# Kernel tuning notes

Measured on AMD Instinct MI355X. Metric: run time of the kernel, lower is better.

The kernel has to match this reference:

```python
import jax, jax.numpy as jnp
import numpy as np

B, S, D, H = 2, 4096, 512, 8
HD = D // H  # head_dim = 64


def _rope_cache(s, d, base=10000.0):
    half = d // 2
    inv_freq = 1.0 / base ** (jnp.arange(half, dtype=jnp.float32) / half)
    t = jnp.arange(s, dtype=jnp.float32)
    freqs = jnp.einsum('s,d->sd', t, inv_freq)          # [s, half]
    emb = jnp.concatenate([freqs, freqs], axis=-1)      # [s, d]
    return jnp.cos(emb), jnp.sin(emb)


def _rotate_half(x):
    x1, x2 = jnp.split(x, 2, axis=-1)
    return jnp.concatenate([-x2, x1], axis=-1)


def setup_inputs() -> dict:
    key = jax.random.key(0)
    k1, k2, k3 = jax.random.split(key, 3)
    x = jax.random.normal(k1, (B, S, D), dtype=jnp.float32)
    W_qkv = jax.random.normal(k2, (D, 3 * D), dtype=jnp.float32) * (D ** -0.5)
    W_out = jax.random.normal(k3, (D, D), dtype=jnp.float32) * (D ** -0.5)
    # causal mask [B, S, S] (True = attend), exercises the masking branch
    causal = jnp.tril(jnp.ones((S, S), dtype=bool))
    attention_mask = jnp.broadcast_to(causal, (B, S, S))
    return {"x": x, "W_qkv": W_qkv, "W_out": W_out, "attention_mask": attention_mask}


def reference(x, W_qkv, W_out, attention_mask):
    b, s, d = x.shape
    qkv = x @ W_qkv                                     # [b, s, 3d]
    q, k, v = jnp.split(qkv, 3, axis=-1)

    def split_heads(t):
        return t.reshape(b, s, H, HD).transpose(0, 2, 1, 3)  # [b, h, s, hd]

    q, k, v = map(split_heads, (q, k, v))
    cos, sin = _rope_cache(s, HD)                       # [s, hd]
    cos = cos[None, None]                               # [1, 1, s, hd]
    sin = sin[None, None]
    q = q * cos + _rotate_half(q) * sin
    k = k * cos + _rotate_half(k) * sin

    scale = HD ** -0.5
    logits = jnp.einsum('bhid,bhjd->bhij', q, k) * scale
    logits = jnp.where(attention_mask[:, None, :, :], logits, jnp.float32(-1e9))
    attn = jax.nn.softmax(logits, axis=-1)
    out = jnp.einsum('bhij,bhjd->bhid', attn, v)
    out = out.transpose(0, 2, 1, 3).reshape(b, s, d)
    return out @ W_out
```

## Files before the change

kernel.cpp:

```cpp
#include <hip/hip_runtime.h>
#include <hip/hip_bf16.h>

typedef __attribute__((ext_vector_type(8))) short bf16x8;
typedef __attribute__((ext_vector_type(4))) float f32x4;
typedef __attribute__((ext_vector_type(16))) float f32x16;
typedef __attribute__((ext_vector_type(4))) unsigned int u32x4;

#define AS3(p)  ((__attribute__((address_space(3))) unsigned int*)(p))
#define AS1C(p) ((const __attribute__((address_space(1))) unsigned int*)(p))

__device__ __forceinline__ ushort f2b(float f){
  __hip_bfloat16 h = __float2bfloat16(f);
  return *reinterpret_cast<ushort*>(&h);
}
__device__ __forceinline__ float b2f(ushort u){
  unsigned int x = ((unsigned int)u) << 16;
  return __uint_as_float(x);
}
__device__ __forceinline__ unsigned int packbf(float lo, float hi){
  return ((unsigned int)f2b(hi) << 16) | (unsigned int)f2b(lo);
}

__device__ __forceinline__ int sniff_f32(const ushort* __restrict__ x, int flat){
  int l = flat & 63;
  float a = b2f(x[l]),     b = b2f(x[l+64]);
  float c = b2f(x[l+128]), d = b2f(x[l+192]);
  int bad = (!(fabsf(a) < 1e6f)) || (!(fabsf(b) < 1e6f)) ||
            (!(fabsf(c) < 1e6f)) || (!(fabsf(d) < 1e6f));
  return __ballot(bad) != 0ULL;
}

__global__ __launch_bounds__(256) void prep(
    const void* __restrict__ x, ushort* __restrict__ xb,
    const void* __restrict__ Wqkv, ushort* __restrict__ WqkvT,
    const void* __restrict__ Wout, ushort* __restrict__ WoutT,
    float* __restrict__ tc, float* __restrict__ ts){
  __shared__ ushort t[32][33];
  const int bid = blockIdx.x, tid = threadIdx.x;
  if (bid < 512){
    int i = bid*256 + tid;
    int s = i >> 5, d = i & 31;
    float inv = powf(10000.0f, -(float)d * (1.0f/32.0f));
    float a = (float)s * inv;
    tc[i] = cosf(a);
    ts[i] = sinf(a);
  } else if (bid < 2560){
    const int isf = sniff_f32((const ushort*)x, tid);
    const int n = 2*4096*512;
    int i = (bid-512)*256 + tid;
    const int stride = 2048*256;
    if (isf){ const float* s = (const float*)x;  for (; i<n; i+=stride) xb[i] = f2b(s[i]); }
    else    { const ushort* s = (const ushort*)x; for (; i<n; i+=stride) xb[i] = s[i]; }
  } else {
    const int isf = sniff_f32((const ushort*)x, tid);
    const void* in; ushort* out; int R, C, bx, by;
    if (bid < 3328){ int q = bid-2560; in = Wqkv; out = WqkvT; R = 512; C = 1536; bx = q%48; by = q/48; }
    else           { int q = bid-3328; in = Wout; out = WoutT; R = 512; C = 512;  bx = q%16; by = q/16; }
    int c0 = bx*32, r0 = by*32;
    int tx = tid&31, ty = tid>>5;
#pragma unroll
    for (int r=0;r<32;r+=8){
      size_t idx = (size_t)(r0+ty+r)*C + c0+tx;
      t[ty+r][tx] = isf ? f2b(((const float*)in)[idx]) : ((const ushort*)in)[idx];
    }
    __syncthreads();
#pragma unroll
    for (int r=0;r<32;r+=8) out[(size_t)(c0+ty+r)*R + r0+tx] = t[tx][ty+r];
  }
}

__global__ __launch_bounds__(256, 2) void qkv_rope(
    const ushort* __restrict__ X, const ushort* __restrict__ WT,
    const float* __restrict__ tc, const float* __restrict__ ts,
    ushort* __restrict__ Q, ushort* __restrict__ Ko, ushort* __restrict__ VT){
  __shared__ __align__(16) ushort Al[128*64];
  __shared__ __align__(16) ushort Bl[128*64];
  __shared__ __align__(16) ushort Tl[64*136];
  const int w = threadIdx.x>>6, lane = threadIdx.x&63;
  const int n0 = blockIdx.x*128, m0 = blockIdx.y*128;
  f32x4 acc[4][4] = {};
  const ushort* Ag = X  + (size_t)m0*512;
  const ushort* Bg = WT + (size_t)n0*512;
  const int srow = lane>>3, sphys = lane&7;
  for (int k0=0;k0<512;k0+=64){
#pragma unroll
    for (int tt=0;tt<4;tt++){
      int r = tt*32 + w*8 + srow;
      int lc = sphys ^ (r&7);
      __builtin_amdgcn_global_load_lds(AS1C(Ag + (size_t)r*512 + k0 + lc*8), AS3(Al + (tt*32+w*8)*64), 16, 0, 0);
      __builtin_amdgcn_global_load_lds(AS1C(Bg + (size_t)r*512 + k0 + lc*8), AS3(Bl + (tt*32+w*8)*64), 16, 0, 0);
    }
    __syncthreads();
    const int mh = (w>>1)*64, nh = (w&1)*64;
#pragma unroll
    for (int kk=0;kk<2;kk++){
      bf16x8 af[4], bf[4];
#pragma unroll
      for (int mt=0;mt<4;mt++){
        int r = mh + mt*16 + (lane&15);
        int pc = (kk*4 + (lane>>4)) ^ (r&7);
        af[mt] = *(const bf16x8*)(Al + r*64 + pc*8);
      }
#pragma unroll
      for (int nt=0;nt<4;nt++){
        int r = nh + nt*16 + (lane&15);
        int pc = (kk*4 + (lane>>4)) ^ (r&7);
        bf[nt] = *(const bf16x8*)(Bl + r*64 + pc*8);
      }
#pragma unroll
      for (int mt=0;mt<4;mt++)
#pragma unroll
        for (int nt=0;nt<4;nt++)
          acc[mt][nt] = __builtin_amdgcn_mfma_f32_16x16x32_bf16(af[mt], bf[nt], acc[mt][nt], 0,0,0);
    }
    __syncthreads();
  }
  const int c = lane & 15;
  const int rbase = m0 + (w>>1)*64 + (lane>>4)*4;
  if (n0 < 1024){
    const int colbase = n0 + (w&1)*64;
    const int sec = colbase >> 9;
    const int h = (colbase & 511) >> 6;
    const float scale = (sec==0) ? 0.125f : 1.0f;
    ushort* Out = (sec==0) ? Q : Ko;
#pragma unroll
    for (int mt=0;mt<4;mt++){
#pragma unroll
      for (int reg=0;reg<4;reg++){
        int rg = rbase + mt*16 + reg;
        int b = rg>>12, s = rg&4095;
        size_t obase = ((size_t)(b*8+h)*4096 + s)*64;
        const float* tcp = tc + s*32;
        const float* tsp = ts + s*32;
#pragma unroll
        for (int nt=0;nt<2;nt++){
          int d1 = nt*16 + c;
          float cv = tcp[d1], sv = tsp[d1];
          float v1 = acc[mt][nt][reg], v2 = acc[mt][nt+2][reg];
          Out[obase + d1]      = f2b(scale*(v1*cv - v2*sv));
          Out[obase + d1 + 32] = f2b(scale*(v2*cv + v1*sv));
        }
      }
    }
  } else {
    const int M = w>>1, P = w&1;
    const int bb = m0>>12, s0 = m0&4095;
    const int dR = threadIdx.x>>4, sj = threadIdx.x&15;
#pragma unroll
    for (int ph=0; ph<2; ph++){
      if (P == ph){
#pragma unroll
        for (int mt=0;mt<4;mt++)
#pragma unroll
          for (int nt=0;nt<4;nt++){
            ushort4 pk;
            pk.x = f2b(acc[mt][nt][0]);
            pk.y = f2b(acc[mt][nt][1]);
            pk.z = f2b(acc[mt][nt][2]);
            pk.w = f2b(acc[mt][nt][3]);
            *(ushort4*)&Tl[(nt*16+c)*136 + M*64 + mt*16 + (lane>>4)*4] = pk;
          }
      }
      __syncthreads();
      const int hh = ((n0 + ph*64) & 511) >> 6;
      ushort* baseV = VT + ((size_t)(bb*8+hh)*64)*4096 + s0;
#pragma unroll
      for (int pass=0; pass<4; pass++){
        int d = pass*16 + dR;
        *(u32x4*)(baseV + (size_t)d*4096 + sj*8) = *(const u32x4*)&Tl[d*136 + sj*8];
      }
      __syncthreads();
    }
  }
}

__global__ __launch_bounds__(256, 2) void flash_attn(
    const ushort* __restrict__ Q, const ushort* __restrict__ K,
    const ushort* __restrict__ V, ushort* __restrict__ O,
    ushort* __restrict__ Opart, float* __restrict__ Lpart){
  __shared__ __align__(16) ushort Kl[2][128*64];
  __shared__ __align__(16) ushort Vl[2][64*128];
  const int w = threadIdx.x>>6, lane = threadIdx.x&63;
  const int ln = lane&31, half = lane>>5;
  const int z = blockIdx.x;
  const int bh = (z&7)*2 + ((z>>3)&1);
  const int t = z>>4;
  int qi, jlo, jhi, mode, slot = 0;
  if (t < 16){ qi = 15 - t; jlo = 0; jhi = qi; mode = 0; }
  else {
    int u = t - 16; qi = 31 - (u>>1); int hf = u&1;
    int h1 = (qi+1) >> 1;
    jlo = hf ? h1 : 0; jhi = hf ? qi : h1-1; mode = 1;
    slot = (bh*16 + (qi-16))*2 + hf;
  }
  const int q0 = qi*128;
  const int qg = q0 + w*32 + ln;
  const ushort* Qb = Q + (size_t)bh*4096*64;
  const ushort* Kb = K + (size_t)bh*4096*64;
  const ushort* Vb = V + (size_t)bh*4096*64;
  bf16x8 qf[4];
#pragma unroll
  for (int kt=0;kt<4;kt++)
    qf[kt] = *(const bf16x8*)(Qb + (size_t)qg*64 + kt*16 + half*8);
  f32x16 oacc[2] = {};
  float lsum = 0.0f;
  const int krow = lane>>3, kchunk = lane&7;
  const int vrow = lane>>4, vchunk = lane&15;
  auto stage = [&](int j, int b){
    const int k0 = j*128;
    ushort* Kd = &Kl[b][0];
    ushort* Vd = &Vl[b][0];
#pragma unroll
    for (int tt=0;tt<4;tt++){
      int rr = (w*4+tt)*8 + krow;
      int kc = kchunk ^ (rr&7);
      __builtin_amdgcn_global_load_lds(AS1C(Kb + (size_t)(k0+rr)*64 + kc*8),
                                       AS3(Kd + (w*4+tt)*8*64), 16, 0, 0);
      int dd = (w*4+tt)*4 + vrow;
      int vc = vchunk ^ (dd&7);
      __builtin_amdgcn_global_load_lds(AS1C(Vb + (size_t)dd*4096 + k0 + vc*8),
                                       AS3(Vd + (w*4+tt)*4*128), 16, 0, 0);
    }
  };
  stage(jlo, 0);
  int cur = 0;
  for (int j=jlo; j<=jhi; j++){
    __syncthreads();
    if (j < jhi) stage(j+1, cur^1);
    const ushort* Kc = &Kl[cur][0];
    const ushort* Vc = &Vl[cur][0];
    const int k0 = j*128;
    const bool diag = (j==qi);
#pragma unroll
    for (int nt=0;nt<4;nt++){
      f32x16 s_ = {};
#pragma unroll
      for (int kt=0;kt<4;kt++){
        int kr = nt*32+ln;
        int p = (kt*2+half) ^ (kr&7);
        bf16x8 kf = *(const bf16x8*)(Kc + kr*64 + p*8);
        s_ = __builtin_amdgcn_mfma_f32_32x32x16_bf16(kf, qf[kt], s_, 0,0,0);
      }
      float pv[16];
      const int kb = k0 + nt*32 + 4*half;
      if (diag){
#pragma unroll
        for (int qd=0;qd<4;qd++)
#pragma unroll
          for (int e=0;e<4;e++){
            float sv = s_[4*qd+e];
            if ((kb + 8*qd + e) > qg) sv = -1e30f;
            pv[4*qd+e] = __expf(fminf(sv, 30.0f));
          }
      } else {
#pragma unroll
        for (int qd=0;qd<4;qd++)
#pragma unroll
          for (int e=0;e<4;e++)
            pv[4*qd+e] = __expf(fminf(s_[4*qd+e], 30.0f));
      }
      unsigned int qk[8];
#pragma unroll
      for (int qd=0;qd<4;qd++){
        lsum += pv[4*qd] + pv[4*qd+1] + pv[4*qd+2] + pv[4*qd+3];
        qk[2*qd]   = packbf(pv[4*qd],   pv[4*qd+1]);
        qk[2*qd+1] = packbf(pv[4*qd+2], pv[4*qd+3]);
      }
#pragma unroll
      for (int khi=0;khi<2;khi++){
        unsigned int keep0 = half ? qk[4*khi+2] : qk[4*khi+0];
        unsigned int keep1 = half ? qk[4*khi+3] : qk[4*khi+1];
        unsigned int send0 = half ? qk[4*khi+0] : qk[4*khi+2];
        unsigned int send1 = half ? qk[4*khi+1] : qk[4*khi+3];
        unsigned int r0 = (unsigned int)__shfl_xor((int)send0, 32);
        unsigned int r1 = (unsigned int)__shfl_xor((int)send1, 32);
        union { unsigned int u[4]; bf16x8 v; } pf;
        pf.u[0] = half ? r0 : keep0;
        pf.u[1] = half ? r1 : keep1;
        pf.u[2] = half ? keep0 : r0;
        pf.u[3] = half ? keep1 : r1;
        const int cl = (nt*2+khi)*2 + half;
#pragma unroll
        for (int dt=0;dt<2;dt++){
          int vr = dt*32+ln;
          int p = cl ^ (vr&7);
          bf16x8 vf = *(const bf16x8*)(Vc + vr*128 + p*8);
          oacc[dt] = __builtin_amdgcn_mfma_f32_32x32x16_bf16(pf.v, vf, oacc[dt], 0,0,0);
        }
      }
    }
    cur ^= 1;
  }
  if (mode == 0){
    float linv = 1.0f / (lsum + __shfl_xor(lsum, 32));
    const int b = bh>>3, h = bh&7;
#pragma unroll
    for (int reg=0;reg<16;reg++){
      int qlocal = (reg&3) + 8*(reg>>2) + 4*half;
      float li = __shfl(linv, qlocal);
      int srw = q0 + w*32 + qlocal;
#pragma unroll
      for (int dt=0;dt<2;dt++)
        O[((size_t)(b*4096+srw))*512 + h*64 + dt*32 + ln] = f2b(oacc[dt][reg]*li);
    }
  } else {
    ushort* Ob = Opart + (size_t)slot*8192;
#pragma unroll
    for (int reg=0;reg<16;reg++){
      int qlocal = (reg&3) + 8*(reg>>2) + 4*half;
      int r = w*32 + qlocal;
#pragma unroll
      for (int dt=0;dt<2;dt++)
        Ob[r*64 + dt*32 + ln] = f2b(oacc[dt][reg]);
    }
    float lrow = lsum + __shfl_xor(lsum, 32);
    if (half == 0) Lpart[slot*128 + w*32 + ln] = lrow;
  }
}

__global__ __launch_bounds__(256) void combine(
    const ushort* __restrict__ Opart, const float* __restrict__ Lpart,
    ushort* __restrict__ O){
  const int qq = blockIdx.x;
  const int bh = blockIdx.y;
  const int slot0 = (bh*16 + qq)*2;
  const ushort* O1 = Opart + (size_t)slot0*8192;
  const ushort* O2 = O1 + 8192;
  const float*  L1 = Lpart + slot0*128;
  const float*  L2 = L1 + 128;
  const int b = bh>>3, h = bh&7;
  const int s0 = (16+qq)*128;
  const int r0 = threadIdx.x>>2, cg = (threadIdx.x&3)*16;
#pragma unroll
  for (int it=0; it<2; it++){
    int r = r0 + it*64;
    float li = 1.0f / (L1[r] + L2[r]);
    ushort* dst = O + ((size_t)(b*4096 + s0 + r))*512 + h*64 + cg;
    const ushort* p1 = O1 + r*64 + cg;
    const ushort* p2 = O2 + r*64 + cg;
#pragma unroll
    for (int e=0;e<16;e++)
      dst[e] = f2b((b2f(p1[e]) + b2f(p2[e])) * li);
  }
}

__global__ __launch_bounds__(256, 2) void out_proj(
    const ushort* __restrict__ A, const ushort* __restrict__ WT,
    void* __restrict__ Out, const ushort* __restrict__ xs){
  __shared__ __align__(16) ushort Al[128*64];
  __shared__ __align__(16) ushort Bl[128*64];
  const int isf = sniff_f32(xs, threadIdx.x);
  const int w = threadIdx.x>>6, lane = threadIdx.x&63;
  const int n0 = blockIdx.x*128, m0 = blockIdx.y*128;
  f32x4 acc[4][4] = {};
  const ushort* Ag = A  + (size_t)m0*512;
  const ushort* Bg = WT + (size_t)n0*512;
  const int srow = lane>>3, sphys = lane&7;
  for (int k0=0;k0<512;k0+=64){
#pragma unroll
    for (int tt=0;tt<4;tt++){
      int r = tt*32 + w*8 + srow;
      int lc = sphys ^ (r&7);
      __builtin_amdgcn_global_load_lds(AS1C(Ag + (size_t)r*512 + k0 + lc*8), AS3(Al + (tt*32+w*8)*64), 16, 0, 0);
      __builtin_amdgcn_global_load_lds(AS1C(Bg + (size_t)r*512 + k0 + lc*8), AS3(Bl + (tt*32+w*8)*64), 16, 0, 0);
    }
    __syncthreads();
    const int mh = (w>>1)*64, nh = (w&1)*64;
#pragma unroll
    for (int kk=0;kk<2;kk++){
      bf16x8 af[4], bf[4];
#pragma unroll
      for (int mt=0;mt<4;mt++){
        int r = mh + mt*16 + (lane&15);
        int pc = (kk*4 + (lane>>4)) ^ (r&7);
        af[mt] = *(const bf16x8*)(Al + r*64 + pc*8);
      }
#pragma unroll
      for (int nt=0;nt<4;nt++){
        int r = nh + nt*16 + (lane&15);
        int pc = (kk*4 + (lane>>4)) ^ (r&7);
        bf[nt] = *(const bf16x8*)(Bl + r*64 + pc*8);
      }
#pragma unroll
      for (int mt=0;mt<4;mt++)
#pragma unroll
        for (int nt=0;nt<4;nt++)
          acc[mt][nt] = __builtin_amdgcn_mfma_f32_16x16x32_bf16(af[mt], bf[nt], acc[mt][nt], 0,0,0);
    }
    __syncthreads();
  }
  const int c = lane&15;
  const int rbase = m0 + (w>>1)*64 + (lane>>4)*4;
  const int cb = n0 + (w&1)*64;
#pragma unroll
  for (int mt=0;mt<4;mt++)
#pragma unroll
    for (int nt=0;nt<4;nt++)
#pragma unroll
      for (int reg=0;reg<4;reg++){
        int rg = rbase + mt*16 + reg;
        size_t idx = (size_t)rg*512 + cb + nt*16 + c;
        float v = acc[mt][nt][reg];
        if (isf) ((float*)Out)[idx] = v;
        else     ((ushort*)Out)[idx] = f2b(v);
      }
}

extern "C" void kernel_launch(void* const* d_in, const int* in_sizes, int n_in,
                              void* d_out, int out_size, void* d_ws, size_t ws_size,
                              hipStream_t stream){
  const void* x    = d_in[0];
  const void* Wqkv = d_in[1];
  const void* Wout = d_in[2];
  char* ws = (char*)d_ws;
  float*  tc    = (float*) (ws + 4096);
  float*  tsn   = (float*) (ws + 528384);
  ushort* WqkvT = (ushort*)(ws + 1052672);
  ushort* WoutT = (ushort*)(ws + 2625536);
  ushort* xb    = (ushort*)(ws + 3149824);
  ushort* Qw    = (ushort*)(ws + 11538432);
  ushort* Kw    = (ushort*)(ws + 19927040);
  ushort* Vw    = (ushort*)(ws + 28315648);
  ushort* Ow    = (ushort*)(ws + 36704256);
  ushort* Opart = xb;
  float*  Lpart = tc;

  prep     <<<dim3(3584),  dim3(256), 0, stream>>>(x, xb, Wqkv, WqkvT, Wout, WoutT, tc, tsn);
  qkv_rope <<<dim3(12,64), dim3(256), 0, stream>>>(xb, WqkvT, tc, tsn, Qw, Kw, Vw);
  flash_attn<<<dim3(768),  dim3(256), 0, stream>>>(Qw, Kw, Vw, Ow, Opart, Lpart);
  combine  <<<dim3(16,16), dim3(256), 0, stream>>>(Opart, Lpart, Ow);
  out_proj <<<dim3(4,64),  dim3(256), 0, stream>>>(Ow, WoutT, d_out, (const ushort*)x);
}
```

Baseline: 288.3 us.

## Compute RoPE inline, shrink attention KV tiles, use exp2 softmax, raise occupancy

Drops the precomputed cos/sin tables and instead evaluates RoPE in the QKV epilogue with hardware sin/cos on fractional turns. Folds log2(e) into the Q scale so the softmax can use exp2 without clamping. Halves the flash-attention K/V tile to 64 keys, which cuts LDS use and allows a higher occupancy hint, and the P operand no longer needs cross-lane shuffles. The bf16 pack now uses a simpler rounding path, and launch bounds are raised on the GEMMs. The risks are register spills from the higher occupancy targets, twice as many loop iterations, and slightly different rounding in the RoPE angles and the packed probabilities.

```diff
diff --git a/kernel.cpp b/kernel.cpp
--- a/kernel.cpp
+++ b/kernel.cpp
@@ -17,8 +17,10 @@
   unsigned int x = ((unsigned int)u) << 16;
   return __uint_as_float(x);
 }
-__device__ __forceinline__ unsigned int packbf(float lo, float hi){
-  return ((unsigned int)f2b(hi) << 16) | (unsigned int)f2b(lo);
+__device__ __forceinline__ unsigned int pack_rn(float lo, float hi){
+  unsigned int a = __float_as_uint(lo) + 0x8000u;
+  unsigned int b = __float_as_uint(hi) + 0x8000u;
+  return __builtin_amdgcn_perm(b, a, 0x07060302u);
 }
 
 __device__ __forceinline__ int sniff_f32(const ushort* __restrict__ x, int flat){
@@ -33,29 +35,21 @@
 __global__ __launch_bounds__(256) void prep(
     const void* __restrict__ x, ushort* __restrict__ xb,
     const void* __restrict__ Wqkv, ushort* __restrict__ WqkvT,
-    const void* __restrict__ Wout, ushort* __restrict__ WoutT,
-    float* __restrict__ tc, float* __restrict__ ts){
+    const void* __restrict__ Wout, ushort* __restrict__ WoutT){
   __shared__ ushort t[32][33];
   const int bid = blockIdx.x, tid = threadIdx.x;
-  if (bid < 512){
-    int i = bid*256 + tid;
-    int s = i >> 5, d = i & 31;
-    float inv = powf(10000.0f, -(float)d * (1.0f/32.0f));
-    float a = (float)s * inv;
-    tc[i] = cosf(a);
-    ts[i] = sinf(a);
-  } else if (bid < 2560){
+  if (bid < 2048){
     const int isf = sniff_f32((const ushort*)x, tid);
     const int n = 2*4096*512;
-    int i = (bid-512)*256 + tid;
+    int i = bid*256 + tid;
     const int stride = 2048*256;
     if (isf){ const float* s = (const float*)x;  for (; i<n; i+=stride) xb[i] = f2b(s[i]); }
     else    { const ushort* s = (const ushort*)x; for (; i<n; i+=stride) xb[i] = s[i]; }
   } else {
     const int isf = sniff_f32((const ushort*)x, tid);
     const void* in; ushort* out; int R, C, bx, by;
-    if (bid < 3328){ int q = bid-2560; in = Wqkv; out = WqkvT; R = 512; C = 1536; bx = q%48; by = q/48; }
-    else           { int q = bid-3328; in = Wout; out = WoutT; R = 512; C = 512;  bx = q%16; by = q/16; }
+    if (bid < 2816){ int q = bid-2048; in = Wqkv; out = WqkvT; R = 512; C = 1536; bx = q%48; by = q/48; }
+    else           { int q = bid-2816; in = Wout; out = WoutT; R = 512; C = 512;  bx = q%16; by = q/16; }
     int c0 = bx*32, r0 = by*32;
     int tx = tid&31, ty = tid>>5;
 #pragma unroll
@@ -69,9 +63,8 @@
   }
 }
 
-__global__ __launch_bounds__(256, 2) void qkv_rope(
+__global__ __launch_bounds__(256, 3) void qkv_rope(
     const ushort* __restrict__ X, const ushort* __restrict__ WT,
-    const float* __restrict__ tc, const float* __restrict__ ts,
     ushort* __restrict__ Q, ushort* __restrict__ Ko, ushort* __restrict__ VT){
   __shared__ __align__(16) ushort Al[128*64];
   __shared__ __align__(16) ushort Bl[128*64];
@@ -121,8 +114,12 @@
     const int colbase = n0 + (w&1)*64;
     const int sec = colbase >> 9;
     const int h = (colbase & 511) >> 6;
-    const float scale = (sec==0) ? 0.125f : 1.0f;
+    const float scale = (sec==0) ? 0.125f*1.44269504089f : 1.0f;
     ushort* Out = (sec==0) ? Q : Ko;
+    float invr[2];
+#pragma unroll
+    for (int nt=0;nt<2;nt++)
+      invr[nt] = __builtin_amdgcn_exp2f(-0.415241011861f * (float)(nt*16 + c)) * 0.159154943092f;
 #pragma unroll
     for (int mt=0;mt<4;mt++){
 #pragma unroll
@@ -130,12 +127,13 @@
         int rg = rbase + mt*16 + reg;
         int b = rg>>12, s = rg&4095;
         size_t obase = ((size_t)(b*8+h)*4096 + s)*64;
-        const float* tcp = tc + s*32;
-        const float* tsp = ts + s*32;
+        float sf = (float)s;
 #pragma unroll
         for (int nt=0;nt<2;nt++){
+          float fr = __builtin_amdgcn_fractf(sf * invr[nt]);
+          float cv = __builtin_amdgcn_cosf(fr);
+          float sv = __builtin_amdgcn_sinf(fr);
           int d1 = nt*16 + c;
-          float cv = tcp[d1], sv = tsp[d1];
           float v1 = acc[mt][nt][reg], v2 = acc[mt][nt+2][reg];
           Out[obase + d1]      = f2b(scale*(v1*cv - v2*sv));
           Out[obase + d1 + 32] = f2b(scale*(v2*cv + v1*sv));
@@ -174,23 +172,22 @@
   }
 }
 
-__global__ __launch_bounds__(256, 2) void flash_attn(
+__global__ __launch_bounds__(256, 4) void flash_attn(
     const ushort* __restrict__ Q, const ushort* __restrict__ K,
     const ushort* __restrict__ V, ushort* __restrict__ O,
     ushort* __restrict__ Opart, float* __restrict__ Lpart){
-  __shared__ __align__(16) ushort Kl[2][128*64];
-  __shared__ __align__(16) ushort Vl[2][64*128];
+  __shared__ __align__(16) ushort Kl[2][64*64];
+  __shared__ __align__(16) ushort Vl[2][64*64];
   const int w = threadIdx.x>>6, lane = threadIdx.x&63;
   const int ln = lane&31, half = lane>>5;
   const int z = blockIdx.x;
   const int bh = (z&7)*2 + ((z>>3)&1);
   const int t = z>>4;
   int qi, jlo, jhi, mode, slot = 0;
-  if (t < 16){ qi = 15 - t; jlo = 0; jhi = qi; mode = 0; }
+  if (t < 16){ qi = 15 - t; jlo = 0; jhi = 2*qi+1; mode = 0; }
   else {
     int u = t - 16; qi = 31 - (u>>1); int hf = u&1;
-    int h1 = (qi+1) >> 1;
-    jlo = hf ? h1 : 0; jhi = hf ? qi : h1-1; mode = 1;
+    jlo = hf ? (qi+1) : 0; jhi = hf ? (2*qi+1) : qi; mode = 1;
     slot = (bh*16 + (qi-16))*2 + hf;
   }
   const int q0 = qi*128;
@@ -204,22 +201,19 @@
     qf[kt] = *(const bf16x8*)(Qb + (size_t)qg*64 + kt*16 + half*8);
   f32x16 oacc[2] = {};
   float lsum = 0.0f;
-  const int krow = lane>>3, kchunk = lane&7;
-  const int vrow = lane>>4, vchunk = lane&15;
+  const int r8 = lane>>3, sl = lane&7;
   auto stage = [&](int j, int b){
-    const int k0 = j*128;
+    const int k0 = j*64;
     ushort* Kd = &Kl[b][0];
     ushort* Vd = &Vl[b][0];
 #pragma unroll
-    for (int tt=0;tt<4;tt++){
-      int rr = (w*4+tt)*8 + krow;
-      int kc = kchunk ^ (rr&7);
-      __builtin_amdgcn_global_load_lds(AS1C(Kb + (size_t)(k0+rr)*64 + kc*8),
-                                       AS3(Kd + (w*4+tt)*8*64), 16, 0, 0);
-      int dd = (w*4+tt)*4 + vrow;
-      int vc = vchunk ^ (dd&7);
-      __builtin_amdgcn_global_load_lds(AS1C(Vb + (size_t)dd*4096 + k0 + vc*8),
-                                       AS3(Vd + (w*4+tt)*4*128), 16, 0, 0);
+    for (int tt=0;tt<2;tt++){
+      int rr = w*16 + tt*8 + r8;
+      int lc = sl ^ (rr&7);
+      __builtin_amdgcn_global_load_lds(AS1C(Kb + (size_t)(k0+rr)*64 + lc*8),
+                                       AS3(Kd + (w*16+tt*8)*64), 16, 0, 0);
+      __builtin_amdgcn_global_load_lds(AS1C(Vb + (size_t)rr*4096 + k0 + lc*8),
+                                       AS3(Vd + (w*16+tt*8)*64), 16, 0, 0);
     }
   };
   stage(jlo, 0);
@@ -229,10 +223,10 @@
     if (j < jhi) stage(j+1, cur^1);
     const ushort* Kc = &Kl[cur][0];
     const ushort* Vc = &Vl[cur][0];
-    const int k0 = j*128;
-    const bool diag = (j==qi);
-#pragma unroll
-    for (int nt=0;nt<4;nt++){
+    const int k0 = j*64;
+    const bool dm = (k0 + 63) > (q0 + w*32);
+#pragma unroll
+    for (int nt=0;nt<2;nt++){
       f32x16 s_ = {};
 #pragma unroll
       for (int kt=0;kt<4;kt++){
@@ -241,51 +235,40 @@
         bf16x8 kf = *(const bf16x8*)(Kc + kr*64 + p*8);
         s_ = __builtin_amdgcn_mfma_f32_32x32x16_bf16(kf, qf[kt], s_, 0,0,0);
       }
+      const int kb = k0 + nt*32 + 4*half;
       float pv[16];
-      const int kb = k0 + nt*32 + 4*half;
-      if (diag){
-#pragma unroll
-        for (int qd=0;qd<4;qd++)
-#pragma unroll
-          for (int e=0;e<4;e++){
-            float sv = s_[4*qd+e];
-            if ((kb + 8*qd + e) > qg) sv = -1e30f;
-            pv[4*qd+e] = __expf(fminf(sv, 30.0f));
-          }
+      if (dm){
+#pragma unroll
+        for (int r=0;r<16;r++){
+          int kk = kb + 8*(r>>2) + (r&3);
+          pv[r] = (kk > qg) ? 0.0f : __builtin_amdgcn_exp2f(s_[r]);
+        }
       } else {
 #pragma unroll
-        for (int qd=0;qd<4;qd++)
-#pragma unroll
-          for (int e=0;e<4;e++)
-            pv[4*qd+e] = __expf(fminf(s_[4*qd+e], 30.0f));
+        for (int r=0;r<16;r++) pv[r] = __builtin_amdgcn_exp2f(s_[r]);
       }
       unsigned int qk[8];
 #pragma unroll
       for (int qd=0;qd<4;qd++){
-        lsum += pv[4*qd] + pv[4*qd+1] + pv[4*qd+2] + pv[4*qd+3];
-        qk[2*qd]   = packbf(pv[4*qd],   pv[4*qd+1]);
-        qk[2*qd+1] = packbf(pv[4*qd+2], pv[4*qd+3]);
+        lsum += (pv[4*qd]+pv[4*qd+1]) + (pv[4*qd+2]+pv[4*qd+3]);
+        qk[2*qd]   = pack_rn(pv[4*qd],   pv[4*qd+1]);
+        qk[2*qd+1] = pack_rn(pv[4*qd+2], pv[4*qd+3]);
       }
 #pragma unroll
       for (int khi=0;khi<2;khi++){
-        unsigned int keep0 = half ? qk[4*khi+2] : qk[4*khi+0];
-        unsigned int keep1 = half ? qk[4*khi+3] : qk[4*khi+1];
-        unsigned int send0 = half ? qk[4*khi+0] : qk[4*khi+2];
-        unsigned int send1 = half ? qk[4*khi+1] : qk[4*khi+3];
-        unsigned int r0 = (unsigned int)__shfl_xor((int)send0, 32);
-        unsigned int r1 = (unsigned int)__shfl_xor((int)send1, 32);
         union { unsigned int u[4]; bf16x8 v; } pf;
-        pf.u[0] = half ? r0 : keep0;
-        pf.u[1] = half ? r1 : keep1;
-        pf.u[2] = half ? keep0 : r0;
-        pf.u[3] = half ? keep1 : r1;
-        const int cl = (nt*2+khi)*2 + half;
+        pf.u[0] = qk[khi*4+0]; pf.u[1] = qk[khi*4+1];
+        pf.u[2] = qk[khi*4+2]; pf.u[3] = qk[khi*4+3];
+        const int c0 = nt*4 + khi*2;
 #pragma unroll
         for (int dt=0;dt<2;dt++){
           int vr = dt*32+ln;
-          int p = cl ^ (vr&7);
-          bf16x8 vf = *(const bf16x8*)(Vc + vr*128 + p*8);
-          oacc[dt] = __builtin_amdgcn_mfma_f32_32x32x16_bf16(pf.v, vf, oacc[dt], 0,0,0);
+          int pc0 = c0 ^ (vr&7);
+          int pc1 = (c0+1) ^ (vr&7);
+          union { unsigned int u[4]; bf16x8 v; } vf;
+          *(uint2*)&vf.u[0] = *(const uint2*)(Vc + vr*64 + pc0*8 + half*4);
+          *(uint2*)&vf.u[2] = *(const uint2*)(Vc + vr*64 + pc1*8 + half*4);
+          oacc[dt] = __builtin_amdgcn_mfma_f32_32x32x16_bf16(pf.v, vf.v, oacc[dt], 0,0,0);
         }
       }
     }
@@ -344,7 +327,7 @@
   }
 }
 
-__global__ __launch_bounds__(256, 2) void out_proj(
+__global__ __launch_bounds__(256, 4) void out_proj(
     const ushort* __restrict__ A, const ushort* __restrict__ WT,
     void* __restrict__ Out, const ushort* __restrict__ xs){
   __shared__ __align__(16) ushort Al[128*64];
@@ -413,8 +396,7 @@
   const void* Wqkv = d_in[1];
   const void* Wout = d_in[2];
   char* ws = (char*)d_ws;
-  float*  tc    = (float*) (ws + 4096);
-  float*  tsn   = (float*) (ws + 528384);
+  float*  Lpart = (float*) (ws + 4096);
   ushort* WqkvT = (ushort*)(ws + 1052672);
   ushort* WoutT = (ushort*)(ws + 2625536);
   ushort* xb    = (ushort*)(ws + 3149824);
@@ -423,10 +405,9 @@
   ushort* Vw    = (ushort*)(ws + 28315648);
   ushort* Ow    = (ushort*)(ws + 36704256);
   ushort* Opart = xb;
-  float*  Lpart = tc;
-
-  prep     <<<dim3(3584),  dim3(256), 0, stream>>>(x, xb, Wqkv, WqkvT, Wout, WoutT, tc, tsn);
-  qkv_rope <<<dim3(12,64), dim3(256), 0, stream>>>(xb, WqkvT, tc, tsn, Qw, Kw, Vw);
+
+  prep     <<<dim3(3072),  dim3(256), 0, stream>>>(x, xb, Wqkv, WqkvT, Wout, WoutT);
+  qkv_rope <<<dim3(12,64), dim3(256), 0, stream>>>(xb, WqkvT, Qw, Kw, Vw);
   flash_attn<<<dim3(768),  dim3(256), 0, stream>>>(Qw, Kw, Vw, Ow, Opart, Lpart);
   combine  <<<dim3(16,16), dim3(256), 0, stream>>>(Opart, Lpart, Ow);
   out_proj <<<dim3(4,64),  dim3(256), 0, stream>>>(Ow, WoutT, d_out, (const ushort*)x);
```

Result: faster. 279.7 us (-3.0%).
